# Performance work log

Measured on AMD Instinct MI355X. Metric: run time of the kernel, lower is better.

Reference implementation:

```python
import jax, jax.numpy as jnp
import numpy as np

# Detector / Siddon constants (from init_kwargs)
H, W = 200, 200
DELX, DELY = 1.5, 1.5
NXV, NYV, NZV = 256, 256, 256  # voxel counts
EPS = 1e-8


def setup_inputs() -> dict:
    key = jax.random.key(0)
    kvol, = jax.random.split(key, 1)
    volume = jax.random.uniform(kvol, (NXV, NYV, NZV), dtype=jnp.float32)  # CT intensities
    spacing = jnp.ones((3,), jnp.float32)                                  # 1mm isotropic
    sdr = jnp.array([300.0], jnp.float32)                                  # source-to-detector radius
    rotations = jnp.array([[0.5, -0.2, 0.3]], jnp.float32)                 # theta, phi, gamma
    translations = jnp.array([[128.0, 128.0, 128.0]], jnp.float32)         # volume center (bx,by,bz)
    return {"volume": volume, "spacing": spacing, "sdr": sdr,
            "rotations": rotations, "translations": translations}


def _rotation_matrix(rotations):
    # R = Rz(theta) @ Ry(phi) @ Rx(gamma), batched
    theta, phi, gamma = rotations[:, 0], rotations[:, 1], rotations[:, 2]
    ct, st = jnp.cos(theta), jnp.sin(theta)
    cp, sp = jnp.cos(phi), jnp.sin(phi)
    cg, sg = jnp.cos(gamma), jnp.sin(gamma)
    z = jnp.zeros_like(theta)
    o = jnp.ones_like(theta)
    Rz = jnp.stack([ct, -st, z, st, ct, z, z, z, o], -1).reshape(-1, 3, 3)
    Ry = jnp.stack([cp, z, sp, z, o, z, -sp, z, cp], -1).reshape(-1, 3, 3)
    Rx = jnp.stack([o, z, z, z, cg, -sg, z, sg, cg], -1).reshape(-1, 3, 3)
    return Rz @ Ry @ Rx


def _make_xrays(sdr, rotations, translations):
    # Detector.make_xrays: source on column 0 of sdr*R, detector center opposite,
    # detector plane spanned by unit columns 1 and 2.
    R = _rotation_matrix(rotations)                 # (b,3,3), orthonormal columns
    source = sdr[:, None] * R[..., 0]               # (b,3)
    center = -source
    basis = jnp.stack([R[..., 1], R[..., 2]], 1)    # (b,2,3)
    source = source + translations
    center = center + translations
    t = (jnp.arange(-(H // 2), H // 2, dtype=jnp.float32) + 1.0) * DELX
    s = (jnp.arange(-(W // 2), W // 2, dtype=jnp.float32) + 1.0) * DELY
    coefs = jnp.stack(jnp.meshgrid(t, s, indexing="ij"), -1).reshape(-1, 2)  # (H*W,2) == cartesian_prod(t,s)
    target = jnp.einsum("bcd,nc->bnd", basis, coefs) + center[:, None, :]    # (b,n,3)
    return source[:, None, :], target               # (b,1,3), (b,n,3)


def reference(volume, spacing, sdr, rotations, translations):
    source, target = _make_xrays(sdr, rotations, translations)
    vol = jnp.flip(volume, 0)                       # Siddon flips axis 0
    nx, ny, nz = vol.shape
    sdd = target - source + EPS                     # (b,n,3) ray directions

    # Alphas at every axis-aligned plane intersection: P = (nx+1)+(ny+1)+(nz+1)
    alphas = jnp.concatenate(
        [(jnp.arange(n + 1, dtype=jnp.float32) * spacing[i] - source[..., i:i + 1]) / sdd[..., i:i + 1]
         for i, n in enumerate((nx, ny, nz))], axis=-1)          # (b,n,P)

    # Entry/exit alphas of the volume bounding box
    extent = jnp.asarray([nx, ny, nz], jnp.float32) * spacing
    a0 = (0.0 - source) / sdd
    a1 = (extent - source) / sdd
    amin = jnp.max(jnp.minimum(a0, a1), -1, keepdims=True)       # (b,n,1)
    amax = jnp.min(jnp.maximum(a0, a1), -1, keepdims=True)

    # Out-of-range alphas -> sentinel amax (sorts to the end, contributes zero step;
    # equivalent to the original's NaN + nansum handling)
    valid = (alphas >= amin) & (alphas <= amax)
    alphas = jnp.sort(jnp.where(valid, alphas, amax), axis=-1)

    mid = 0.5 * (alphas[..., :-1] + alphas[..., 1:])             # (b,n,P-1)
    step = jnp.diff(alphas, axis=-1)

    # Midpoint positions -> voxel indices (trunc, clamped in-bounds)
    xyz = source[:, :, None, :] + mid[..., None] * sdd[:, :, None, :]  # (b,n,P-1,3)
    idx = jnp.trunc(xyz / spacing).astype(jnp.int32)
    ix = jnp.clip(idx[..., 0], 0, nx - 1)
    iy = jnp.clip(idx[..., 1], 0, ny - 1)
    iz = jnp.clip(idx[..., 2], 0, nz - 1)
    voxels = vol[ix, iy, iz]                                     # gather, (b,n,P-1)

    drr = jnp.sum(voxels * step, -1) * jnp.linalg.norm(sdd, axis=-1)
    return drr.reshape(-1, H, W)
```

## Files before the change

### kernel.cpp

```cpp
#include <hip/hip_runtime.h>

#define H_ 200
#define W_ 200
#define DELX_ 1.5f
#define DELY_ 1.5f
#define NXV_ 256
#define NYV_ 256
#define NZV_ 256
#define EPS_ 1e-8f
#define NSEG 16
#define SEGS_PER_BLK 8
#define TILE_R 4
#define TILE_C 16
#define TROWS (H_ / TILE_R)
#define TCOLS ((W_ + TILE_C - 1) / TILE_C)
#define TILES_PER_IMG (TROWS * TCOLS)
#define G_ 8
#define MAXG 10

__device__ __forceinline__ float alpha_mul(float k, float sp, float src, float inv_sdd) {
    return (k * sp - src) * inv_sdd;
}

__global__ void __launch_bounds__(512, 8)
drr_partial(const float* __restrict__ vol,
            const float* __restrict__ spacing,
            const float* __restrict__ sdr,
            const float* __restrict__ rot,
            const float* __restrict__ trans,
            float* __restrict__ partials,
            int npix) {
    const int t = threadIdx.x;
    const int pixLocal = t & 63;
    const int half = blockIdx.x & 1;
    const int seg = (t >> 6) + (half << 3);
    const int tileBlk = blockIdx.x >> 1;

    const int b    = tileBlk / TILES_PER_IMG;
    const int rem  = tileBlk % TILES_PER_IMG;
    const int ty   = rem / TCOLS;
    const int tx   = rem % TCOLS;
    const int i = ty * TILE_R + (pixLocal >> 4);
    const int j = tx * TILE_C + (pixLocal & 15);

    const float theta = rot[b * 3 + 0], phi = rot[b * 3 + 1], gamma = rot[b * 3 + 2];
    const float ct = cosf(theta), st = sinf(theta);
    const float cp = cosf(phi),   sp = sinf(phi);
    const float cg = cosf(gamma), sg = sinf(gamma);
    const float r00 = ct * cp,                r10 = st * cp,                r20 = -sp;
    const float r01 = ct * sp * sg - st * cg, r11 = st * sp * sg + ct * cg, r21 = cp * sg;
    const float r02 = ct * sp * cg + st * sg, r12 = st * sp * cg - ct * sg, r22 = cp * cg;

    const float sd = sdr[b];
    const float tx_ = trans[b * 3 + 0], ty_ = trans[b * 3 + 1], tz_ = trans[b * 3 + 2];
    const float sx = sd * r00 + tx_, sy = sd * r10 + ty_, sz = sd * r20 + tz_;
    const float cxx = -sd * r00 + tx_, cyy = -sd * r10 + ty_, czz = -sd * r20 + tz_;

    const float tco = ((float)(i - H_ / 2) + 1.0f) * DELX_;
    const float sco = ((float)(j - W_ / 2) + 1.0f) * DELY_;
    const float gx = r01 * tco + r02 * sco + cxx;
    const float gy = r11 * tco + r12 * sco + cyy;
    const float gz = r21 * tco + r22 * sco + czz;

    const float dx = gx - sx + EPS_;
    const float dy = gy - sy + EPS_;
    const float dz = gz - sz + EPS_;

    const float spx = spacing[0], spy = spacing[1], spz = spacing[2];
    const float inv_spx = 1.0f / spx, inv_spy = 1.0f / spy, inv_spz = 1.0f / spz;
    const float inv_dx = 1.0f / dx, inv_dy = 1.0f / dy, inv_dz = 1.0f / dz;

    const float a0x = alpha_mul(0.f, spx, sx, inv_dx), a1x = alpha_mul((float)NXV_, spx, sx, inv_dx);
    const float a0y = alpha_mul(0.f, spy, sy, inv_dy), a1y = alpha_mul((float)NYV_, spy, sy, inv_dy);
    const float a0z = alpha_mul(0.f, spz, sz, inv_dz), a1z = alpha_mul((float)NZV_, spz, sz, inv_dz);

    const float amin = fmaxf(fmaxf(fminf(a0x, a1x), fminf(a0y, a1y)), fminf(a0z, a1z));
    const float amax = fminf(fminf(fmaxf(a0x, a1x), fmaxf(a0y, a1y)), fmaxf(a0z, a1z));

    const float norm = sqrtf(dx * dx + dy * dy + dz * dz);

    const float klo = (float)(seg * (NXV_ / NSEG));
    const float khi = (float)((seg + 1) * (NXV_ / NSEG));
    const float aA = alpha_mul(klo, spx, sx, inv_dx);
    const float aB = alpha_mul(khi, spx, sx, inv_dx);
    const float lo = fminf(aA, aB), hi = fmaxf(aA, aB);

    const float start = fmaxf(amin, lo);
    const float end   = fminf(amax, hi);

    float acc = 0.0f;
    if (start < end) {
        float kx, ky, kz, axv, ayv, azv, dkx, dky, dkz;
        {
            float kf = (start * dx + sx) * inv_spx;
            if (dx > 0.f) { dkx = 1.f;  kx = floorf(kf) + 1.f; }
            else          { dkx = -1.f; kx = ceilf(kf) - 1.f; }
            axv = alpha_mul(kx, spx, sx, inv_dx);
        }
        {
            float kf = (start * dy + sy) * inv_spy;
            if (dy > 0.f) { dky = 1.f;  ky = floorf(kf) + 1.f; }
            else          { dky = -1.f; ky = ceilf(kf) - 1.f; }
            ayv = alpha_mul(ky, spy, sy, inv_dy);
        }
        {
            float kf = (start * dz + sz) * inv_spz;
            if (dz > 0.f) { dkz = 1.f;  kz = floorf(kf) + 1.f; }
            else          { dkz = -1.f; kz = ceilf(kf) - 1.f; }
            azv = alpha_mul(kz, spz, sz, inv_dz);
        }

        int off_cur;
        {
            float an0 = fminf(axv, fminf(ayv, azv));
            float midv = 0.5f * (start + an0);
            int ix = (int)((sx + midv * dx) * inv_spx);
            int iy = (int)((sy + midv * dy) * inv_spy);
            int iz = (int)((sz + midv * dz) * inv_spz);
            ix = min(max(ix, 0), NXV_ - 1);
            iy = min(max(iy, 0), NYV_ - 1);
            iz = min(max(iz, 0), NZV_ - 1);
            off_cur = ((NXV_ - 1 - ix) * NYV_ + iy) * NZV_ + iz;
        }
        const int doffx = (dkx > 0.f) ? -(NYV_ * NZV_) : (NYV_ * NZV_);
        const int doffy = (dky > 0.f) ? NZV_ : -NZV_;
        const int doffz = (dkz > 0.f) ? 1 : -1;

        float a_cur = start;
        for (int g = 0; g < MAXG; ++g) {
            float stp[G_];
            int   off[G_];
            float an_last;
            #pragma unroll
            for (int u = 0; u < G_; ++u) {
                float an = fminf(axv, fminf(ayv, azv));
                bool ok = (an <= end);
                stp[u] = ok ? (an - a_cur) : 0.0f;
                off[u] = off_cur;
                a_cur = an;
                bool upd = (an < end);
                bool cx = (axv == an), cy = (ayv == an), cz = (azv == an);
                kx = cx ? kx + dkx : kx;
                ky = cy ? ky + dky : ky;
                kz = cz ? kz + dkz : kz;
                off_cur += ((cx && upd) ? doffx : 0)
                         + ((cy && upd) ? doffy : 0)
                         + ((cz && upd) ? doffz : 0);
                axv = alpha_mul(kx, spx, sx, inv_dx);
                ayv = alpha_mul(ky, spy, sy, inv_dy);
                azv = alpha_mul(kz, spz, sz, inv_dz);
                an_last = an;
            }
            float v[G_];
            #pragma unroll
            for (int u = 0; u < G_; ++u) v[u] = vol[off[u]];
            #pragma unroll
            for (int u = 0; u < G_; ++u) acc += v[u] * stp[u];
            if (an_last > end) break;
        }
    }
    float result = acc * norm;

    __shared__ float red[SEGS_PER_BLK * 64];
    red[t] = result;
    __syncthreads();
    if (t < 64) {
        const int ii = ty * TILE_R + (t >> 4);
        const int jj = tx * TILE_C + (t & 15);
        if (jj < W_) {
            const int opix = b * (H_ * W_) + ii * W_ + jj;
            float s = 0.0f;
            #pragma unroll
            for (int k = 0; k < SEGS_PER_BLK; k++) s += red[t + k * 64];
            partials[(size_t)half * npix + opix] = s;
        }
    }
}

__global__ void __launch_bounds__(256)
drr_combine(const float* __restrict__ partials, float* __restrict__ out, int npix) {
    int pix = blockIdx.x * blockDim.x + threadIdx.x;
    if (pix >= npix) return;
    out[pix] = partials[pix] + partials[(size_t)npix + pix];
}

extern "C" void kernel_launch(void* const* d_in, const int* in_sizes, int n_in,
                              void* d_out, int out_size, void* d_ws, size_t ws_size,
                              hipStream_t stream) {
    const float* vol     = (const float*)d_in[0];
    const float* spacing = (const float*)d_in[1];
    const float* sdr     = (const float*)d_in[2];
    const float* rot     = (const float*)d_in[3];
    const float* trans   = (const float*)d_in[4];
    float* out = (float*)d_out;

    const int B = in_sizes[2];
    const int npix = B * H_ * W_;
    float* partials = (float*)d_ws;

    const int nblocks = B * TILES_PER_IMG * 2;
    drr_partial<<<nblocks, 64 * SEGS_PER_BLK, 0, stream>>>(vol, spacing, sdr, rot, trans, partials, npix);
    drr_combine<<<(npix + 255) / 256, 256, 0, stream>>>(partials, out, npix);
}
```

Measured before the change: 117.7 us.

## Software-pipeline ray march so gathers overlap computation of the next group

Splits the Siddon traversal into double-buffered groups, so the volume gathers for one group of 8 crossings are issued before the next group's alpha/offset stepping is computed. The goal is to hide gather latency behind ALU work. Loop exit now uses a wave-wide __all vote, so all lanes keep going until every lane has passed the segment end. Launch bounds drop from 8 to 6 blocks per CU to allow more registers for the extra buffers, at the cost of occupancy.

```diff
diff --git a/kernel.cpp b/kernel.cpp
--- a/kernel.cpp
+++ b/kernel.cpp
@@ -22,7 +22,28 @@
     return (k * sp - src) * inv_sdd;
 }
 
-__global__ void __launch_bounds__(512, 8)
+#define MARCH(OFF, STP)                                                       \
+    _Pragma("unroll")                                                         \
+    for (int u = 0; u < G_; ++u) {                                            \
+        float an = fminf(axv, fminf(ayv, azv));                               \
+        bool ok = (an <= aend);                                               \
+        STP[u] = ok ? (an - a_cur) : 0.0f;                                    \
+        OFF[u] = off_cur;                                                     \
+        a_cur = an;                                                           \
+        bool upd = (an < aend);                                               \
+        bool cx = (axv == an), cy = (ayv == an), cz = (azv == an);            \
+        kx = cx ? kx + dkx : kx;                                              \
+        ky = cy ? ky + dky : ky;                                              \
+        kz = cz ? kz + dkz : kz;                                              \
+        off_cur += ((cx && upd) ? doffx : 0)                                  \
+                 + ((cy && upd) ? doffy : 0)                                  \
+                 + ((cz && upd) ? doffz : 0);                                 \
+        axv = alpha_mul(kx, spx, sx, inv_dx);   \
+        ayv = alpha_mul(ky, spy, sy, inv_dy);                                 \
+        azv = alpha_mul(kz, spz, sz, inv_dz);                                 \
+    }
+
+__global__ void __launch_bounds__(512, 6)
 drr_partial(const float* __restrict__ vol,
             const float* __restrict__ spacing,
             const float* __restrict__ sdr,
@@ -86,10 +107,10 @@
     const float lo = fminf(aA, aB), hi = fmaxf(aA, aB);
 
     const float start = fmaxf(amin, lo);
-    const float end   = fminf(amax, hi);
+    const float aend  = fminf(amax, hi);
 
     float acc = 0.0f;
-    if (start < end) {
+    if (start < aend) {
         float kx, ky, kz, axv, ayv, azv, dkx, dky, dkz;
         {
             float kf = (start * dx + sx) * inv_spx;
@@ -127,36 +148,27 @@
         const int doffz = (dkz > 0.f) ? 1 : -1;
 
         float a_cur = start;
-        for (int g = 0; g < MAXG; ++g) {
-            float stp[G_];
-            int   off[G_];
-            float an_last;
-            #pragma unroll
-            for (int u = 0; u < G_; ++u) {
-                float an = fminf(axv, fminf(ayv, azv));
-                bool ok = (an <= end);
-                stp[u] = ok ? (an - a_cur) : 0.0f;
-                off[u] = off_cur;
-                a_cur = an;
-                bool upd = (an < end);
-                bool cx = (axv == an), cy = (ayv == an), cz = (azv == an);
-                kx = cx ? kx + dkx : kx;
-                ky = cy ? ky + dky : ky;
-                kz = cz ? kz + dkz : kz;
-                off_cur += ((cx && upd) ? doffx : 0)
-                         + ((cy && upd) ? doffy : 0)
-                         + ((cz && upd) ? doffz : 0);
-                axv = alpha_mul(kx, spx, sx, inv_dx);
-                ayv = alpha_mul(ky, spy, sy, inv_dy);
-                azv = alpha_mul(kz, spz, sz, inv_dz);
-                an_last = an;
-            }
-            float v[G_];
-            #pragma unroll
-            for (int u = 0; u < G_; ++u) v[u] = vol[off[u]];
-            #pragma unroll
-            for (int u = 0; u < G_; ++u) acc += v[u] * stp[u];
-            if (an_last > end) break;
+        int   offA[G_], offB[G_];
+        float stpA[G_], stpB[G_], v[G_];
+
+        MARCH(offA, stpA);
+        #pragma unroll 1
+        for (int g = 0; g < MAXG; g += 2) {
+            #pragma unroll
+            for (int u = 0; u < G_; ++u) v[u] = vol[offA[u]];
+            const bool moreA = !__all(a_cur > aend);
+            if (moreA) { MARCH(offB, stpB); }
+            #pragma unroll
+            for (int u = 0; u < G_; ++u) acc += v[u] * stpA[u];
+            if (!moreA) break;
+
+            #pragma unroll
+            for (int u = 0; u < G_; ++u) v[u] = vol[offB[u]];
+            const bool moreB = !__all(a_cur > aend);
+            if (moreB) { MARCH(offA, stpA); }
+            #pragma unroll
+            for (int u = 0; u < G_; ++u) acc += v[u] * stpB[u];
+            if (!moreB) break;
         }
     }
     float result = acc * norm;
```

New measurement: 129.6 us. 1.1x slower.

## Remap blocks across XCDs, issue gathers inline, and use wave-uniform loop exit

Applied to the files above, without the earlier changes.

Remaps the block index so that consecutive logical tiles land on the same XCD chiplet, and the two halves are split by range instead of interleaving. The aim is to improve L2 locality of volume gathers within each XCD. Volume loads are now issued inside the traversal loop rather than batched after it. The outer loop is marked not to unroll, and it exits only when every lane in the wave has finished, via __all. This reduces divergent control flow but keeps finished lanes running extra iterations with zero steps.

```diff
diff --git a/kernel.cpp b/kernel.cpp
--- a/kernel.cpp
+++ b/kernel.cpp
@@ -30,11 +30,19 @@
             const float* __restrict__ trans,
             float* __restrict__ partials,
             int npix) {
+    const int nwg = gridDim.x;
+    const int q8 = nwg >> 3, r8 = nwg & 7;
+    const int xcd = blockIdx.x & 7;
+    const int sub = blockIdx.x >> 3;
+    const int wg = (xcd < r8 ? xcd * (q8 + 1) : r8 * (q8 + 1) + (xcd - r8) * q8) + sub;
+
+    const int ntiles = nwg >> 1;
+    const int half    = (wg < ntiles) ? 0 : 1;
+    const int tileBlk = wg - half * ntiles;
+
     const int t = threadIdx.x;
     const int pixLocal = t & 63;
-    const int half = blockIdx.x & 1;
     const int seg = (t >> 6) + (half << 3);
-    const int tileBlk = blockIdx.x >> 1;
 
     const int b    = tileBlk / TILES_PER_IMG;
     const int rem  = tileBlk % TILES_PER_IMG;
@@ -83,13 +91,11 @@
     const float khi = (float)((seg + 1) * (NXV_ / NSEG));
     const float aA = alpha_mul(klo, spx, sx, inv_dx);
     const float aB = alpha_mul(khi, spx, sx, inv_dx);
-    const float lo = fminf(aA, aB), hi = fmaxf(aA, aB);
-
-    const float start = fmaxf(amin, lo);
-    const float end   = fminf(amax, hi);
+    const float start = fmaxf(amin, fminf(aA, aB));
+    const float aend  = fminf(amax, fmaxf(aA, aB));
 
     float acc = 0.0f;
-    if (start < end) {
+    if (start < aend) {
         float kx, ky, kz, axv, ayv, azv, dkx, dky, dkz;
         {
             float kf = (start * dx + sx) * inv_spx;
@@ -127,18 +133,18 @@
         const int doffz = (dkz > 0.f) ? 1 : -1;
 
         float a_cur = start;
+        #pragma unroll 1
         for (int g = 0; g < MAXG; ++g) {
             float stp[G_];
-            int   off[G_];
-            float an_last;
+            float v[G_];
             #pragma unroll
             for (int u = 0; u < G_; ++u) {
                 float an = fminf(axv, fminf(ayv, azv));
-                bool ok = (an <= end);
+                bool ok = (an <= aend);
                 stp[u] = ok ? (an - a_cur) : 0.0f;
-                off[u] = off_cur;
+                v[u] = vol[off_cur];
                 a_cur = an;
-                bool upd = (an < end);
+                bool upd = (an < aend);
                 bool cx = (axv == an), cy = (ayv == an), cz = (azv == an);
                 kx = cx ? kx + dkx : kx;
                 ky = cy ? ky + dky : ky;
@@ -149,14 +155,10 @@
                 axv = alpha_mul(kx, spx, sx, inv_dx);
                 ayv = alpha_mul(ky, spy, sy, inv_dy);
                 azv = alpha_mul(kz, spz, sz, inv_dz);
-                an_last = an;
             }
-            float v[G_];
-            #pragma unroll
-            for (int u = 0; u < G_; ++u) v[u] = vol[off[u]];
             #pragma unroll
             for (int u = 0; u < G_; ++u) acc += v[u] * stp[u];
-            if (an_last > end) break;
+            if (__all(a_cur > aend)) break;
         }
     }
     float result = acc * norm;
```

Measured after the change: 119.9 us. About the same (+1.8%).
